# Performance work log

Hardware: AMD Instinct MI355X
Metric: run time of the kernel (lower is better)

Reference implementation:

```python
import jax, jax.numpy as jnp
import numpy as np

B, T, D, H = 128, 256, 64, 512
MISSING = 128.0  # MISSING_VALUE marker from AJ-RNN repo


def _lstm_params(key, in_dim):
    k1, k2 = jax.random.split(key)
    K = jax.random.normal(k1, (in_dim, 4 * H), jnp.float32) * 0.05
    R = jax.random.normal(k2, (H, 4 * H), jnp.float32) * 0.05
    # Keras LSTMCell: zeros bias with unit forget bias (gate order i, f, c, o)
    b = jnp.concatenate([jnp.zeros((H,)), jnp.ones((H,)), jnp.zeros((2 * H,))]).astype(jnp.float32)
    return K, R, b


def setup_inputs() -> dict:
    key = jax.random.key(0)
    ks = jax.random.split(key, 6)
    x = jax.random.normal(ks[0], (B, T, D), jnp.float32)
    miss = jax.random.uniform(ks[1], (B, T, D)) < 0.2
    x = jnp.where(miss, MISSING, x)  # inject missing-value markers
    k0, r0, b0 = _lstm_params(ks[2], D)   # layer 0: input dim D
    k1, r1, b1 = _lstm_params(ks[3], H)   # layer 1: input dim H
    W = jax.random.normal(ks[4], (H, D), jnp.float32) * 0.1  # imputation kernel
    bias = jnp.full((D,), 0.1, jnp.float32)
    return dict(x=x, k0=k0, r0=r0, b0=b0, k1=k1, r1=r1, b1=b1, W=W, bias=bias)


def _lstm_cell(x, h, c, K, R, b):
    z = x @ K + h @ R + b  # [B, 4H]
    i, f, g, o = jnp.split(z, 4, axis=-1)
    i = jax.nn.sigmoid(i)
    f = jax.nn.sigmoid(f)
    g = jnp.tanh(g)
    o = jax.nn.sigmoid(o)
    c_new = f * c + i * g
    h_new = o * jnp.tanh(c_new)
    return h_new, c_new


def reference(x, k0, r0, b0, k1, r1, b1, W, bias):
    xs = jnp.swapaxes(x, 0, 1)          # [T, B, D]
    flags = jnp.arange(T) > 0           # t==0 uses raw input, no imputation

    def step(carry, inp):
        h1, c1, h2, c2 = carry
        x_t, flag = inp
        pred = h2 @ W + bias            # prediction from previous top-layer output
        cur = jnp.where(flag & (x_t == MISSING), pred, x_t)
        h1, c1 = _lstm_cell(cur, h1, c1, k0, r0, b0)
        h2, c2 = _lstm_cell(h1, h2, c2, k1, r1, b1)
        return (h1, c1, h2, c2), h2

    init = tuple(jnp.zeros((B, H), jnp.float32) for _ in range(4))
    _, outs = jax.lax.scan(step, init, (xs, flags))  # outs: [T, B, H]

    # tf.concat(outputs[:-1], axis=1) then reshape [-1, H] == batch-major, time inner
    hidden = jnp.swapaxes(outs[:-1], 0, 1).reshape(-1, H)  # [B*(T-1), H]
    prediction = hidden @ W + bias                          # [B*(T-1), D]
    last_cell = outs[-1]                                    # [B, H]
    return prediction, last_cell
```

## Files before the change

kernel.cpp:

```cpp
#include <hip/hip_runtime.h>
#include <hip/hip_bf16.h>


typedef __bf16        v8bf  __attribute__((ext_vector_type(8)));
typedef float         f32x4 __attribute__((ext_vector_type(4)));
typedef unsigned int  u32x4 __attribute__((ext_vector_type(4)));

constexpr int B_ = 128, T_ = 256, D_ = 64, H_ = 512;

constexpr size_t OFF_WP1 = 0;
constexpr size_t OFF_WP2 = 2359296;
constexpr size_t OFF_WPP = 6553600;
constexpr size_t OFF_H1G = 6619136;
constexpr size_t OFF_H2G = 6750208;
constexpr size_t OFF_FLG = 6881280;

__device__ __forceinline__ v8bf ldv(const __hip_bfloat16* p) {
  return *reinterpret_cast<const v8bf*>(p);
}
__device__ __forceinline__ f32x4 MF(v8bf a, v8bf b, f32x4 c) {
  return __builtin_amdgcn_mfma_f32_16x16x32_bf16(a, b, c, 0, 0, 0);
}
__device__ __forceinline__ float sigf(float x) { return 1.0f / (1.0f + __expf(-x)); }
__device__ __forceinline__ float tanhfast(float x) {
  x = fminf(15.0f, fmaxf(-15.0f, x));
  float e = __expf(-2.0f * x);
  return (1.0f - e) / (1.0f + e);
}

__device__ __forceinline__ void st_llc_u16(void* p, unsigned v) {
  asm volatile("global_store_short %0, %1, off sc0 sc1" :: "v"(p), "v"(v) : "memory");
}
__device__ __forceinline__ void st_flag(unsigned* p, unsigned v) {
  asm volatile("global_store_dword %0, %1, off sc0 sc1" :: "v"(p), "v"(v) : "memory");
}
__device__ __forceinline__ void vm0() {
  asm volatile("s_waitcnt vmcnt(0)" ::: "memory");
}
__device__ __forceinline__ void ld_llc64_issue(const char* g, u32x4& a, u32x4& b,
                                               u32x4& c, u32x4& d) {
  asm volatile(
      "global_load_dwordx4 %0, %4, off sc0 sc1\n\t"
      "global_load_dwordx4 %1, %4, off offset:16 sc0 sc1\n\t"
      "global_load_dwordx4 %2, %4, off offset:32 sc0 sc1\n\t"
      "global_load_dwordx4 %3, %4, off offset:48 sc0 sc1"
      : "=&v"(a), "=&v"(b), "=&v"(c), "=&v"(d)
      : "v"(g)
      : "memory");
}
__device__ __forceinline__ void poll_flags(const unsigned* fbase, int lane,
                                           unsigned tgt) {
  const unsigned* fp = fbase + (lane & 31);
  for (;;) {
    unsigned f;
    asm volatile("global_load_dword %0, %1, off sc0 sc1\n\ts_waitcnt vmcnt(0)"
                 : "=v"(f) : "v"(fp) : "memory");
    if (!__any((int)(f < tgt))) return;
  }
}

__global__ __launch_bounds__(256) void pack_weights(
    const float* __restrict__ kp, const float* __restrict__ rp,
    int krows, int ncols, int nkc, int nct, __hip_bfloat16* __restrict__ out) {
  int tid = blockIdx.x * 256 + threadIdx.x;
  int total = nct * nkc * 64;
  if (tid >= total) return;
  int L  = tid & 63;
  int kc = (tid >> 6) % nkc;
  int ct = tid / (64 * nkc);
  int n  = ct * 16 + (L & 15);
  int kb = kc * 32 + (L >> 4) * 8;
  __hip_bfloat16* dst = out + (size_t)tid * 8;
#pragma unroll
  for (int j = 0; j < 8; ++j) {
    int kk = kb + j;
    float v = (kk < krows) ? kp[kk * ncols + n] : rp[(kk - krows) * ncols + n];
    dst[j] = __float2bfloat16(v);
  }
}

__global__ __launch_bounds__(256) void init_state(unsigned* __restrict__ flg) {
  int idx = blockIdx.x * 256 + threadIdx.x;
  if (idx < 512) flg[idx] = 0u;
}

__global__ __launch_bounds__(256, 1) void rnn_persist(
    const float* __restrict__ x,
    const __hip_bfloat16* __restrict__ Wp1,
    const __hip_bfloat16* __restrict__ Wp2,
    const __hip_bfloat16* __restrict__ WpP,
    const float* __restrict__ b0,
    const float* __restrict__ b1,
    const float* __restrict__ biasD,
    __hip_bfloat16* __restrict__ h1g,
    __hip_bfloat16* __restrict__ h2g,
    unsigned* __restrict__ flg,
    float* __restrict__ pred_out,
    float* __restrict__ last_out) {

  __shared__ alignas(16) __hip_bfloat16 h1P[16][512];
  __shared__ alignas(16) __hip_bfloat16 h1Q[16][512];
  __shared__ alignas(16) __hip_bfloat16 h2L[16][512];
  __shared__ alignas(16) __hip_bfloat16 curL[16][72];
  __shared__ float zb[4][16][17];

  const int tid = threadIdx.x;
  const int rg = blockIdx.x & 7;
  const int cg = blockIdx.x >> 3;
  const int w  = tid >> 6;
  const int L  = tid & 63;
  const int m  = L & 15;
  const int q  = L >> 4;
  const int row2 = tid >> 4;
  const int col2 = tid & 15;
  const int C  = cg * 16 + col2;
  const int R  = rg * 16 + row2;
  const int sw = (m & 7) << 3;

  const int so0 = col2 * 64;
  const int ssw = (row2 & 7) << 4;
  const size_t gso = (size_t)row2 * 1024 + so0;

  v8bf wpp[16], wp1[18], wp2[32];
  {
    const int ct = w * 32 + cg;
#pragma unroll
    for (int kc = 0; kc < 16; ++kc)
      wpp[kc] = ldv(WpP + ((size_t)(w * 16 + kc) * 64 + L) * 8);
#pragma unroll
    for (int kc = 0; kc < 18; ++kc)
      wp1[kc] = ldv(Wp1 + ((size_t)(ct * 18 + kc) * 64 + L) * 8);
#pragma unroll
    for (int kc = 0; kc < 32; ++kc)
      wp2[kc] = ldv(Wp2 + ((size_t)(ct * 32 + kc) * 64 + L) * 8);
  }
  const float b0i = b0[C], b0f = b0[512 + C], b0g = b0[1024 + C], b0o = b0[1536 + C];
  const float b1i = b1[C], b1f = b1[512 + C], b1g = b1[1024 + C], b1o = b1[1536 + C];
  const float bD  = biasD[w * 16 + m];

  float c1v = 0.0f, c2v = 0.0f;

  const size_t rgbase = (size_t)rg * 16 * H_;
  unsigned* fbase = flg + (rg << 6);
  const int hidx = R * H_ + C;
  const int prow0 = rg * 16 + q * 4;
  const int pcol  = w * 16 + m;

  {
    u32x4 zz = {0u, 0u, 0u, 0u};
    u32x4* p1 = reinterpret_cast<u32x4*>(&h1P[0][0]);
    u32x4* p2 = reinterpret_cast<u32x4*>(&h2L[0][0]);
#pragma unroll
    for (int i = 0; i < 4; ++i) { p1[tid * 4 + i] = zz; p2[tid * 4 + i] = zz; }
  }
  __syncthreads();

  for (int t = 0; t < T_; ++t) {
    __hip_bfloat16 (*h1L)[512] = (t & 1) ? h1Q : h1P;
    __hip_bfloat16 (*h1N)[512] = (t & 1) ? h1P : h1Q;

    f32x4 z1a = {0.f,0.f,0.f,0.f}, z1b = {0.f,0.f,0.f,0.f};
#pragma unroll
    for (int c = 0; c < 8; c += 2) {
      v8bf a0 = ldv(&h1L[m][(c * 32 + q * 8) ^ sw]);
      v8bf a1 = ldv(&h1L[m][((c + 1) * 32 + q * 8) ^ sw]);
      z1a = MF(a0, wp1[2 + c], z1a);
      z1b = MF(a1, wp1[3 + c], z1b);
    }

    if (t > 0 && w == 0) poll_flags(fbase, L, 2u * (unsigned)t);
    __syncthreads();

    u32x4 sa, sb, sc2, sd;
    if (t > 0)
      ld_llc64_issue((const char*)(h2g + rgbase) + gso, sa, sb, sc2, sd);
#pragma unroll
    for (int c = 8; c < 16; c += 2) {
      v8bf a0 = ldv(&h1L[m][(c * 32 + q * 8) ^ sw]);
      v8bf a1 = ldv(&h1L[m][((c + 1) * 32 + q * 8) ^ sw]);
      z1a = MF(a0, wp1[2 + c], z1a);
      z1b = MF(a1, wp1[3 + c], z1b);
    }
    if (t > 0) {
      vm0();
      char* lb = (char*)(&h2L[row2][0]);
      *(u32x4*)(lb + ((so0 +  0) ^ ssw)) = sa;
      *(u32x4*)(lb + ((so0 + 16) ^ ssw)) = sb;
      *(u32x4*)(lb + ((so0 + 32) ^ ssw)) = sc2;
      *(u32x4*)(lb + ((so0 + 48) ^ ssw)) = sd;
    }
    __syncthreads();

    {
      f32x4 a0 = {0.f,0.f,0.f,0.f};
      if (t > 0) {
        f32x4 a1 = {0.f,0.f,0.f,0.f};
#pragma unroll
        for (int kc = 0; kc < 16; kc += 2) {
          v8bf x0 = ldv(&h2L[m][(kc * 32 + q * 8) ^ sw]);
          v8bf x1 = ldv(&h2L[m][((kc + 1) * 32 + q * 8) ^ sw]);
          a0 = MF(x0, wpp[kc], a0);
          a1 = MF(x1, wpp[kc + 1], a1);
        }
        a0 += a1;
      }
#pragma unroll
      for (int r = 0; r < 4; ++r) {
        const int rowl = prow0 + r;
        const float xf = x[((size_t)rowl * T_ + t) * D_ + pcol];
        float pv = a0[r] + bD;
        const bool missv = (t > 0) && (xf == 128.0f);
        curL[q * 4 + r][pcol] = __float2bfloat16(missv ? pv : xf);
        if (cg == 0 && t > 0)
          pred_out[((size_t)rowl * (T_ - 1) + (t - 1)) * D_ + pcol] = pv;
      }
    }
    __syncthreads();

    {
      v8bf a0 = ldv(&curL[m][q * 8]);
      v8bf a1 = ldv(&curL[m][32 + q * 8]);
      z1a = MF(a0, wp1[0], z1a);
      z1b = MF(a1, wp1[1], z1b);
      f32x4 zf = z1a + z1b;
#pragma unroll
      for (int r = 0; r < 4; ++r) zb[w][q * 4 + r][m] = zf[r];
    }
    __syncthreads();

    {
      float iv = zb[0][row2][col2] + b0i;
      float fv = zb[1][row2][col2] + b0f;
      float gv = zb[2][row2][col2] + b0g;
      float ov = zb[3][row2][col2] + b0o;
      float ig = sigf(iv), fg = sigf(fv), gg = tanhfast(gv), og = sigf(ov);
      c1v = fg * c1v + ig * gg;
      float hn = og * tanhfast(c1v);
      st_llc_u16(&h1g[hidx], (unsigned)__builtin_bit_cast(unsigned short,
                                                          __float2bfloat16(hn)));
    }
    vm0();
    __syncthreads();
    if (tid == 0) st_flag(fbase + cg, 2u * (unsigned)t + 1u);

    f32x4 z2a = {0.f,0.f,0.f,0.f}, z2b = {0.f,0.f,0.f,0.f};
#pragma unroll
    for (int c = 0; c < 8; c += 2) {
      v8bf a0 = ldv(&h2L[m][(c * 32 + q * 8) ^ sw]);
      v8bf a1 = ldv(&h2L[m][((c + 1) * 32 + q * 8) ^ sw]);
      z2a = MF(a0, wp2[16 + c], z2a);
      z2b = MF(a1, wp2[17 + c], z2b);
    }
    if (w == 0) poll_flags(fbase, L, 2u * (unsigned)t + 1u);
    __syncthreads();

    ld_llc64_issue((const char*)(h1g + rgbase) + gso, sa, sb, sc2, sd);
#pragma unroll
    for (int c = 8; c < 16; c += 2) {
      v8bf a0 = ldv(&h2L[m][(c * 32 + q * 8) ^ sw]);
      v8bf a1 = ldv(&h2L[m][((c + 1) * 32 + q * 8) ^ sw]);
      z2a = MF(a0, wp2[16 + c], z2a);
      z2b = MF(a1, wp2[17 + c], z2b);
    }
    vm0();
    {
      char* lb = (char*)(&h1N[row2][0]);
      *(u32x4*)(lb + ((so0 +  0) ^ ssw)) = sa;
      *(u32x4*)(lb + ((so0 + 16) ^ ssw)) = sb;
      *(u32x4*)(lb + ((so0 + 32) ^ ssw)) = sc2;
      *(u32x4*)(lb + ((so0 + 48) ^ ssw)) = sd;
    }
    __syncthreads();

    {
#pragma unroll
      for (int c = 0; c < 16; c += 2) {
        v8bf a0 = ldv(&h1N[m][(c * 32 + q * 8) ^ sw]);
        v8bf a1 = ldv(&h1N[m][((c + 1) * 32 + q * 8) ^ sw]);
        z2a = MF(a0, wp2[c], z2a);
        z2b = MF(a1, wp2[c + 1], z2b);
      }
      f32x4 zf = z2a + z2b;
#pragma unroll
      for (int r = 0; r < 4; ++r) zb[w][q * 4 + r][m] = zf[r];
    }
    __syncthreads();

    {
      float iv = zb[0][row2][col2] + b1i;
      float fv = zb[1][row2][col2] + b1f;
      float gv = zb[2][row2][col2] + b1g;
      float ov = zb[3][row2][col2] + b1o;
      float ig = sigf(iv), fg = sigf(fv), gg = tanhfast(gv), og = sigf(ov);
      c2v = fg * c2v + ig * gg;
      float hn = og * tanhfast(c2v);
      if (t == T_ - 1) {
        last_out[hidx] = hn;
      } else {
        st_llc_u16(&h2g[hidx], (unsigned)__builtin_bit_cast(unsigned short,
                                                            __float2bfloat16(hn)));
      }
    }
    if (t == T_ - 1) break;
    vm0();
    __syncthreads();
    if (tid == 0) st_flag(fbase + cg, 2u * (unsigned)t + 2u);
  }
}

extern "C" void kernel_launch(void* const* d_in, const int* in_sizes, int n_in,
                              void* d_out, int out_size, void* d_ws, size_t ws_size,
                              hipStream_t stream) {
  const float* x    = (const float*)d_in[0];
  const float* k0   = (const float*)d_in[1];
  const float* r0   = (const float*)d_in[2];
  const float* b0   = (const float*)d_in[3];
  const float* k1   = (const float*)d_in[4];
  const float* r1   = (const float*)d_in[5];
  const float* b1   = (const float*)d_in[6];
  const float* W    = (const float*)d_in[7];
  const float* bias = (const float*)d_in[8];

  char* ws = (char*)d_ws;
  __hip_bfloat16* Wp1 = (__hip_bfloat16*)(ws + OFF_WP1);
  __hip_bfloat16* Wp2 = (__hip_bfloat16*)(ws + OFF_WP2);
  __hip_bfloat16* WpP = (__hip_bfloat16*)(ws + OFF_WPP);
  __hip_bfloat16* h1g = (__hip_bfloat16*)(ws + OFF_H1G);
  __hip_bfloat16* h2g = (__hip_bfloat16*)(ws + OFF_H2G);
  unsigned*       flg = (unsigned*)(ws + OFF_FLG);

  pack_weights<<<(128 * 18 * 64 + 255) / 256, 256, 0, stream>>>(k0, r0, 64, 2048, 18, 128, Wp1);
  pack_weights<<<(128 * 32 * 64 + 255) / 256, 256, 0, stream>>>(k1, r1, 512, 2048, 32, 128, Wp2);
  pack_weights<<<(4 * 16 * 64 + 255) / 256, 256, 0, stream>>>(W, W, 512, 64, 16, 4, WpP);
  init_state<<<2, 256, 0, stream>>>(flg);

  float* outp = (float*)d_out;
  float* last = outp + (size_t)B_ * (T_ - 1) * D_;

  rnn_persist<<<256, 256, 0, stream>>>(x, Wp1, Wp2, WpP, b0, b1, bias,
                                       h1g, h2g, flg, outp, last);
}
```

Baseline: 1.752 ms.

## Replace per-block flag polling with atomic counters and overlap more MFMA with waits

Swaps the per-block flag array, which one wave polled with a 32-lane load, for a single atomic counter per row group. Each block increments it and waiters spin on an atomic load with s_sleep. More of the recurrent MFMA work is moved ahead of the barriers (the first h1 chunk is computed before the flag increment), so latency hides behind the cross-block wait. The x load and prediction store are also vectorised to float4 via an LDS staging buffer. The risk is atomic contention on one counter per row group, and that reordering the signal after extra compute could delay consumers.

```diff
diff --git a/kernel.cpp b/kernel.cpp
--- a/kernel.cpp
+++ b/kernel.cpp
@@ -30,9 +30,6 @@
 
 __device__ __forceinline__ void st_llc_u16(void* p, unsigned v) {
   asm volatile("global_store_short %0, %1, off sc0 sc1" :: "v"(p), "v"(v) : "memory");
-}
-__device__ __forceinline__ void st_flag(unsigned* p, unsigned v) {
-  asm volatile("global_store_dword %0, %1, off sc0 sc1" :: "v"(p), "v"(v) : "memory");
 }
 __device__ __forceinline__ void vm0() {
   asm volatile("s_waitcnt vmcnt(0)" ::: "memory");
@@ -47,16 +44,6 @@
       : "=&v"(a), "=&v"(b), "=&v"(c), "=&v"(d)
       : "v"(g)
       : "memory");
-}
-__device__ __forceinline__ void poll_flags(const unsigned* fbase, int lane,
-                                           unsigned tgt) {
-  const unsigned* fp = fbase + (lane & 31);
-  for (;;) {
-    unsigned f;
-    asm volatile("global_load_dword %0, %1, off sc0 sc1\n\ts_waitcnt vmcnt(0)"
-                 : "=v"(f) : "v"(fp) : "memory");
-    if (!__any((int)(f < tgt))) return;
-  }
 }
 
 __global__ __launch_bounds__(256) void pack_weights(
@@ -102,6 +89,7 @@
   __shared__ alignas(16) __hip_bfloat16 h1Q[16][512];
   __shared__ alignas(16) __hip_bfloat16 h2L[16][512];
   __shared__ alignas(16) __hip_bfloat16 curL[16][72];
+  __shared__ alignas(16) float predb[16][68];
   __shared__ float zb[4][16][17];
 
   const int tid = threadIdx.x;
@@ -115,6 +103,7 @@
   const int col2 = tid & 15;
   const int C  = cg * 16 + col2;
   const int R  = rg * 16 + row2;
+  const int c0 = col2 * 4;
   const int sw = (m & 7) << 3;
 
   const int so0 = col2 * 64;
@@ -141,10 +130,10 @@
   float c1v = 0.0f, c2v = 0.0f;
 
   const size_t rgbase = (size_t)rg * 16 * H_;
-  unsigned* fbase = flg + (rg << 6);
+  const float* xrow = x + (size_t)R * T_ * D_;
+  float* prow = pred_out + (size_t)R * (T_ - 1) * D_;
+  unsigned* cnt = flg + rg * 64;
   const int hidx = R * H_ + C;
-  const int prow0 = rg * 16 + q * 4;
-  const int pcol  = w * 16 + m;
 
   {
     u32x4 zz = {0u, 0u, 0u, 0u};
@@ -155,27 +144,33 @@
   }
   __syncthreads();
 
+  f32x4 z1a = {0.f,0.f,0.f,0.f}, z1b = {0.f,0.f,0.f,0.f};
+
   for (int t = 0; t < T_; ++t) {
     __hip_bfloat16 (*h1L)[512] = (t & 1) ? h1Q : h1P;
     __hip_bfloat16 (*h1N)[512] = (t & 1) ? h1P : h1Q;
 
-    f32x4 z1a = {0.f,0.f,0.f,0.f}, z1b = {0.f,0.f,0.f,0.f};
-#pragma unroll
-    for (int c = 0; c < 8; c += 2) {
+    const float4 xv = *reinterpret_cast<const float4*>(xrow + t * D_ + c0);
+
+#pragma unroll
+    for (int c = 8; c < 12; c += 2) {
       v8bf a0 = ldv(&h1L[m][(c * 32 + q * 8) ^ sw]);
       v8bf a1 = ldv(&h1L[m][((c + 1) * 32 + q * 8) ^ sw]);
       z1a = MF(a0, wp1[2 + c], z1a);
       z1b = MF(a1, wp1[3 + c], z1b);
     }
-
-    if (t > 0 && w == 0) poll_flags(fbase, L, 2u * (unsigned)t);
+    if (t > 0 && tid < 64) {
+      const unsigned tgt = 64u * (unsigned)t;
+      while (__hip_atomic_load(cnt, __ATOMIC_RELAXED, __HIP_MEMORY_SCOPE_AGENT) < tgt)
+        __builtin_amdgcn_s_sleep(1);
+    }
     __syncthreads();
 
     u32x4 sa, sb, sc2, sd;
     if (t > 0)
       ld_llc64_issue((const char*)(h2g + rgbase) + gso, sa, sb, sc2, sd);
 #pragma unroll
-    for (int c = 8; c < 16; c += 2) {
+    for (int c = 12; c < 16; c += 2) {
       v8bf a0 = ldv(&h1L[m][(c * 32 + q * 8) ^ sw]);
       v8bf a1 = ldv(&h1L[m][((c + 1) * 32 + q * 8) ^ sw]);
       z1a = MF(a0, wp1[2 + c], z1a);
@@ -191,29 +186,33 @@
     }
     __syncthreads();
 
-    {
-      f32x4 a0 = {0.f,0.f,0.f,0.f};
-      if (t > 0) {
-        f32x4 a1 = {0.f,0.f,0.f,0.f};
-#pragma unroll
-        for (int kc = 0; kc < 16; kc += 2) {
-          v8bf x0 = ldv(&h2L[m][(kc * 32 + q * 8) ^ sw]);
-          v8bf x1 = ldv(&h2L[m][((kc + 1) * 32 + q * 8) ^ sw]);
-          a0 = MF(x0, wpp[kc], a0);
-          a1 = MF(x1, wpp[kc + 1], a1);
-        }
-        a0 += a1;
+    if (t > 0) {
+      f32x4 a0 = {0.f,0.f,0.f,0.f}, a1 = {0.f,0.f,0.f,0.f};
+#pragma unroll
+      for (int kc = 0; kc < 16; kc += 2) {
+        v8bf x0 = ldv(&h2L[m][(kc * 32 + q * 8) ^ sw]);
+        v8bf x1 = ldv(&h2L[m][((kc + 1) * 32 + q * 8) ^ sw]);
+        a0 = MF(x0, wpp[kc], a0);
+        a1 = MF(x1, wpp[kc + 1], a1);
       }
-#pragma unroll
-      for (int r = 0; r < 4; ++r) {
-        const int rowl = prow0 + r;
-        const float xf = x[((size_t)rowl * T_ + t) * D_ + pcol];
-        float pv = a0[r] + bD;
-        const bool missv = (t > 0) && (xf == 128.0f);
-        curL[q * 4 + r][pcol] = __float2bfloat16(missv ? pv : xf);
-        if (cg == 0 && t > 0)
-          pred_out[((size_t)rowl * (T_ - 1) + (t - 1)) * D_ + pcol] = pv;
+      a0 += a1;
+#pragma unroll
+      for (int r = 0; r < 4; ++r) predb[q * 4 + r][w * 16 + m] = a0[r] + bD;
+    }
+    __syncthreads();
+
+    {
+      float4 pv = {0.f, 0.f, 0.f, 0.f};
+      if (t > 0) pv = *reinterpret_cast<const float4*>(&predb[row2][c0]);
+      const float xa[4] = {xv.x, xv.y, xv.z, xv.w};
+      const float pa[4] = {pv.x, pv.y, pv.z, pv.w};
+#pragma unroll
+      for (int j = 0; j < 4; ++j) {
+        const bool missv = (t > 0) && (xa[j] == 128.0f);
+        curL[row2][c0 + j] = __float2bfloat16(missv ? pa[j] : xa[j]);
       }
+      if (cg == 0 && t > 0)
+        *reinterpret_cast<float4*>(prow + (size_t)(t - 1) * D_ + c0) = pv;
     }
     __syncthreads();
 
@@ -228,6 +227,7 @@
     }
     __syncthreads();
 
+    f32x4 z2a = {0.f,0.f,0.f,0.f}, z2b = {0.f,0.f,0.f,0.f};
     {
       float iv = zb[0][row2][col2] + b0i;
       float fv = zb[1][row2][col2] + b0f;
@@ -239,11 +239,6 @@
       st_llc_u16(&h1g[hidx], (unsigned)__builtin_bit_cast(unsigned short,
                                                           __float2bfloat16(hn)));
     }
-    vm0();
-    __syncthreads();
-    if (tid == 0) st_flag(fbase + cg, 2u * (unsigned)t + 1u);
-
-    f32x4 z2a = {0.f,0.f,0.f,0.f}, z2b = {0.f,0.f,0.f,0.f};
 #pragma unroll
     for (int c = 0; c < 8; c += 2) {
       v8bf a0 = ldv(&h2L[m][(c * 32 + q * 8) ^ sw]);
@@ -251,12 +246,28 @@
       z2a = MF(a0, wp2[16 + c], z2a);
       z2b = MF(a1, wp2[17 + c], z2b);
     }
-    if (w == 0) poll_flags(fbase, L, 2u * (unsigned)t + 1u);
+    vm0();
+    __syncthreads();
+    if (tid == 0)
+      __hip_atomic_fetch_add(cnt, 1u, __ATOMIC_RELAXED, __HIP_MEMORY_SCOPE_AGENT);
+
+#pragma unroll
+    for (int c = 8; c < 12; c += 2) {
+      v8bf a0 = ldv(&h2L[m][(c * 32 + q * 8) ^ sw]);
+      v8bf a1 = ldv(&h2L[m][((c + 1) * 32 + q * 8) ^ sw]);
+      z2a = MF(a0, wp2[16 + c], z2a);
+      z2b = MF(a1, wp2[17 + c], z2b);
+    }
+    if (tid < 64) {
+      const unsigned tgt = 32u * (2u * (unsigned)t + 1u);
+      while (__hip_atomic_load(cnt, __ATOMIC_RELAXED, __HIP_MEMORY_SCOPE_AGENT) < tgt)
+        __builtin_amdgcn_s_sleep(1);
+    }
     __syncthreads();
 
     ld_llc64_issue((const char*)(h1g + rgbase) + gso, sa, sb, sc2, sd);
 #pragma unroll
-    for (int c = 8; c < 16; c += 2) {
+    for (int c = 12; c < 16; c += 2) {
       v8bf a0 = ldv(&h2L[m][(c * 32 + q * 8) ^ sw]);
       v8bf a1 = ldv(&h2L[m][((c + 1) * 32 + q * 8) ^ sw]);
       z2a = MF(a0, wp2[16 + c], z2a);
@@ -296,15 +307,24 @@
       float hn = og * tanhfast(c2v);
       if (t == T_ - 1) {
         last_out[hidx] = hn;
-      } else {
-        st_llc_u16(&h2g[hidx], (unsigned)__builtin_bit_cast(unsigned short,
-                                                            __float2bfloat16(hn)));
+        break;
       }
-    }
-    if (t == T_ - 1) break;
+      st_llc_u16(&h2g[hidx], (unsigned)__builtin_bit_cast(unsigned short,
+                                                          __float2bfloat16(hn)));
+    }
+    z1a = (f32x4){0.f,0.f,0.f,0.f};
+    z1b = (f32x4){0.f,0.f,0.f,0.f};
+#pragma unroll
+    for (int c = 0; c < 8; c += 2) {
+      v8bf a0 = ldv(&h1N[m][(c * 32 + q * 8) ^ sw]);
+      v8bf a1 = ldv(&h1N[m][((c + 1) * 32 + q * 8) ^ sw]);
+      z1a = MF(a0, wp1[2 + c], z1a);
+      z1b = MF(a1, wp1[3 + c], z1b);
+    }
     vm0();
     __syncthreads();
-    if (tid == 0) st_flag(fbase + cg, 2u * (unsigned)t + 2u);
+    if (tid == 0)
+      __hip_atomic_fetch_add(cnt, 1u, __ATOMIC_RELAXED, __HIP_MEMORY_SCOPE_AGENT);
   }
 }
 
```

Result: faster. 1.467 ms (-16.3%).
